# Kernel tuning notes

Measured on AMD Instinct MI355X. Metric: run time of the kernel, lower is better.

## Reference

```python
import jax, jax.numpy as jnp
import numpy as np
import math

B, S, D_IN, D_Q = 4, 2048, 512, 512

def setup_inputs() -> dict:
    key = jax.random.key(0)
    ks = jax.random.split(key, 7)
    s_in = 1.0 / math.sqrt(D_IN)
    x = jax.random.normal(ks[0], (B, S, D_IN), dtype=jnp.float32)
    # nn.Linear-style params: W [out,in], b [out]; uniform(-1/sqrt(in), 1/sqrt(in))
    Wq = jax.random.uniform(ks[1], (D_Q, D_IN), jnp.float32, -s_in, s_in)
    bq = jax.random.uniform(ks[2], (D_Q,), jnp.float32, -s_in, s_in)
    Wk = jax.random.uniform(ks[3], (D_Q, D_IN), jnp.float32, -s_in, s_in)
    bk = jax.random.uniform(ks[4], (D_Q,), jnp.float32, -s_in, s_in)
    Wv = jax.random.uniform(ks[5], (D_Q, D_IN), jnp.float32, -s_in, s_in)
    bv = jax.random.uniform(ks[6], (D_Q,), jnp.float32, -s_in, s_in)
    return {"x": x, "Wq": Wq, "bq": bq, "Wk": Wk, "bk": bk, "Wv": Wv, "bv": bv}

def reference(x, Wq, bq, Wk, bk, Wv, bv):
    # Q/K/V projections: [B,S,D_IN] @ W^T + b -> [B,S,D_Q]
    Q = jnp.einsum('bsi,qi->bsq', x, Wq) + bq
    K = jnp.einsum('bsi,qi->bsq', x, Wk) + bk
    V = jnp.einsum('bsi,qi->bsq', x, Wv) + bv
    scale = 1.0 / math.sqrt(D_Q)
    scores = jnp.einsum('bsq,btq->bst', Q, K) * scale  # [B,S,S]
    attention = jax.nn.softmax(scores, axis=-1)        # 'atten_prob'
    weighted = jnp.einsum('bst,btq->bsq', attention, V)  # 'atten_score'
    return (attention, weighted)
```

## Files before the change

kernel.cpp:

```cpp
#include <hip/hip_runtime.h>
#include <hip/hip_bf16.h>

typedef unsigned short u16;
typedef short bf16x8 __attribute__((ext_vector_type(8)));
typedef float f32x4 __attribute__((ext_vector_type(4)));

#define S_LEN 2048
#define DQ 512
#define NBATCH 4

__device__ __forceinline__ u16 f2bf(float f) {
    __hip_bfloat16 h = __float2bfloat16(f);
    return *reinterpret_cast<u16*>(&h);
}
__device__ __forceinline__ float bf2f(u16 u) {
    unsigned v = ((unsigned)u) << 16;
    union { unsigned u; float f; } c; c.u = v; return c.f;
}

__device__ __forceinline__ void async16(const u16* g, u16* l) {
    __builtin_amdgcn_global_load_lds(
        (__attribute__((address_space(1))) void*)g,
        (__attribute__((address_space(3))) void*)l, 16, 0, 0);
}

__device__ __forceinline__ int xcd_swz(int bid, int chunk) {
    return (bid & 7) * chunk + (bid >> 3);
}

__global__ __launch_bounds__(256) void k_cvt_all(const float* __restrict__ x,
                                                 const float* __restrict__ wq,
                                                 const float* __restrict__ wk,
                                                 const float* __restrict__ wv,
                                                 u16* __restrict__ xb, u16* __restrict__ wb,
                                                 float* __restrict__ sums) {
    int bid = blockIdx.x;
    if (bid >= 4864) {
        int i = (bid - 4864) * 256 + threadIdx.x;
        *(f32x4*)(sums + (size_t)i * 4) = (f32x4)0.0f;
        return;
    }
    const float* src;
    u16* dst;
    int i;
    if (bid < 4096)      { src = x;  dst = xb;          i = bid * 256 + threadIdx.x; }
    else if (bid < 4352) { src = wq; dst = wb;          i = (bid - 4096) * 256 + threadIdx.x; }
    else if (bid < 4608) { src = wk; dst = wb + 262144; i = (bid - 4352) * 256 + threadIdx.x; }
    else                 { src = wv; dst = wb + 524288; i = (bid - 4608) * 256 + threadIdx.x; }
    f32x4 v = *(const f32x4*)(src + (size_t)i * 4);
    ushort4 o;
    o.x = f2bf(v.x); o.y = f2bf(v.y); o.z = f2bf(v.z); o.w = f2bf(v.w);
    *(ushort4*)(dst + (size_t)i * 4) = o;
}

__device__ __forceinline__ void stage_unit(const u16* __restrict__ G, u16* buf,
                                           int kcol, int h, int tid) {
#pragma unroll
    for (int q = 0; q < 2; ++q) {
        int c   = q * 512 + tid;
        int r   = c >> 3;
        int p   = c & 7;
        int lch = p ^ (r & 7);
        async16(G + (size_t)(h * 128 + r) * DQ + kcol + lch * 8,
                buf + h * 8192 + c * 8);
    }
}

__device__ __forceinline__ void gemm256(const u16* __restrict__ A, const u16* __restrict__ B,
                                        u16* ldsA, u16* ldsB, f32x4 acc[8][4], int tid) {
    const int lane = tid & 63;
    const int w    = tid >> 6;
    const int wr   = w >> 2;
    const int wc   = w & 3;
    const int l16  = lane & 15;
    const int quad = lane >> 4;
    const int p0   = quad ^ (l16 & 7);
    const int a0   = (wr * 128 + l16) * 64 + p0 * 8;
    const int a1   = (wr * 128 + l16) * 64 + (p0 ^ 4) * 8;
    const int b0   = (wc * 64 + l16) * 64 + p0 * 8;
    const int b1   = (wc * 64 + l16) * 64 + (p0 ^ 4) * 8;

    stage_unit(A, ldsA, 0, 0, tid);
    stage_unit(A, ldsA, 0, 1, tid);
    stage_unit(B, ldsB, 0, 0, tid);
    stage_unit(B, ldsB, 0, 1, tid);
    __syncthreads();

    for (int kt = 0; kt < 8; ++kt) {
        const u16* rdA = ldsA + (kt & 1) * 16384;
        const u16* rdB = ldsB + (kt & 1) * 16384;
        u16* wrA = ldsA + ((kt + 1) & 1) * 16384;
        u16* wrB = ldsB + ((kt + 1) & 1) * 16384;
        const int  kc = (kt + 1) * 64;
        const bool pf = kt < 7;
        bf16x8 a[4][2], bbf[2][2];

        if (pf) stage_unit(A, wrA, kc, 0, tid);
#pragma unroll
        for (int i = 0; i < 4; ++i) {
            a[i][0] = *(const bf16x8*)(rdA + a0 + i * 1024);
            a[i][1] = *(const bf16x8*)(rdA + a1 + i * 1024);
        }
#pragma unroll
        for (int j = 0; j < 2; ++j) {
            bbf[j][0] = *(const bf16x8*)(rdB + b0 + j * 1024);
            bbf[j][1] = *(const bf16x8*)(rdB + b1 + j * 1024);
        }
        __builtin_amdgcn_s_setprio(1);
#pragma unroll
        for (int i = 0; i < 4; ++i)
#pragma unroll
            for (int j = 0; j < 2; ++j) {
                acc[i][j] = __builtin_amdgcn_mfma_f32_16x16x32_bf16(a[i][0], bbf[j][0], acc[i][j], 0, 0, 0);
                acc[i][j] = __builtin_amdgcn_mfma_f32_16x16x32_bf16(a[i][1], bbf[j][1], acc[i][j], 0, 0, 0);
            }
        __builtin_amdgcn_s_setprio(0);

        if (pf) stage_unit(A, wrA, kc, 1, tid);
#pragma unroll
        for (int j = 0; j < 2; ++j) {
            bbf[j][0] = *(const bf16x8*)(rdB + b0 + (2 + j) * 1024);
            bbf[j][1] = *(const bf16x8*)(rdB + b1 + (2 + j) * 1024);
        }
        __builtin_amdgcn_s_setprio(1);
#pragma unroll
        for (int i = 0; i < 4; ++i)
#pragma unroll
            for (int j = 0; j < 2; ++j) {
                acc[i][2 + j] = __builtin_amdgcn_mfma_f32_16x16x32_bf16(a[i][0], bbf[j][0], acc[i][2 + j], 0, 0, 0);
                acc[i][2 + j] = __builtin_amdgcn_mfma_f32_16x16x32_bf16(a[i][1], bbf[j][1], acc[i][2 + j], 0, 0, 0);
            }
        __builtin_amdgcn_s_setprio(0);

        if (pf) stage_unit(B, wrB, kc, 0, tid);
#pragma unroll
        for (int i = 0; i < 4; ++i) {
            a[i][0] = *(const bf16x8*)(rdA + a0 + (4 + i) * 1024);
            a[i][1] = *(const bf16x8*)(rdA + a1 + (4 + i) * 1024);
        }
        __builtin_amdgcn_s_setprio(1);
#pragma unroll
        for (int i = 0; i < 4; ++i)
#pragma unroll
            for (int j = 0; j < 2; ++j) {
                acc[4 + i][2 + j] = __builtin_amdgcn_mfma_f32_16x16x32_bf16(a[i][0], bbf[j][0], acc[4 + i][2 + j], 0, 0, 0);
                acc[4 + i][2 + j] = __builtin_amdgcn_mfma_f32_16x16x32_bf16(a[i][1], bbf[j][1], acc[4 + i][2 + j], 0, 0, 0);
            }
        __builtin_amdgcn_s_setprio(0);

        if (pf) stage_unit(B, wrB, kc, 1, tid);
#pragma unroll
        for (int j = 0; j < 2; ++j) {
            bbf[j][0] = *(const bf16x8*)(rdB + b0 + j * 1024);
            bbf[j][1] = *(const bf16x8*)(rdB + b1 + j * 1024);
        }
        __builtin_amdgcn_s_setprio(1);
#pragma unroll
        for (int i = 0; i < 4; ++i)
#pragma unroll
            for (int j = 0; j < 2; ++j) {
                acc[4 + i][j] = __builtin_amdgcn_mfma_f32_16x16x32_bf16(a[i][0], bbf[j][0], acc[4 + i][j], 0, 0, 0);
                acc[4 + i][j] = __builtin_amdgcn_mfma_f32_16x16x32_bf16(a[i][1], bbf[j][1], acc[4 + i][j], 0, 0, 0);
            }
        __builtin_amdgcn_s_setprio(0);

        __syncthreads();
    }
}

__global__ __launch_bounds__(512, 2) void k_proj(const u16* __restrict__ xb, const u16* __restrict__ Wb,
                                                 const float* __restrict__ bq, const float* __restrict__ bk,
                                                 const float* __restrict__ bv, u16* __restrict__ out,
                                                 u16* __restrict__ VT) {
    __shared__ __align__(16) u16 lds[65536];
    const int l  = xcd_swz(blockIdx.x, 24);
    const int bx = l & 1;
    const int by = (l >> 1) & 31;
    const int z  = l >> 6;
    const int m0 = by * 256, n0 = bx * 256;
    const u16* A = xb + (size_t)m0 * DQ;
    const u16* B = Wb + (size_t)z * DQ * DQ + (size_t)n0 * DQ;
    const float* bias = (z == 0) ? bq : (z == 1) ? bk : bv;

    f32x4 acc[8][4];
#pragma unroll
    for (int i = 0; i < 8; ++i)
#pragma unroll
        for (int j = 0; j < 4; ++j) acc[i][j] = (f32x4)0.0f;

    const int tid = threadIdx.x;
    gemm256(A, B, lds, lds + 32768, acc, tid);

    const int lane = tid & 63, w = tid >> 6;
    const int wr = w >> 2, wc = w & 3;
    const int l16 = lane & 15, quad = lane >> 4;

    if (z < 2) {
        u16* outz = out + (size_t)z * 8192 * DQ;
#pragma unroll
        for (int j = 0; j < 4; ++j) {
            int gn = n0 + wc * 64 + j * 16 + l16;
            float bv_ = bias[gn];
#pragma unroll
            for (int i = 0; i < 8; ++i)
#pragma unroll
                for (int r = 0; r < 4; ++r) {
                    int gm = m0 + wr * 128 + i * 16 + quad * 4 + r;
                    outz[(size_t)gm * DQ + gn] = f2bf(acc[i][j][r] + bv_);
                }
        }
    } else {
        const int bb_ = m0 >> 11;
        u16* VTb_ = VT + (size_t)bb_ * DQ * S_LEN;
#pragma unroll
        for (int j = 0; j < 4; ++j) {
            int gn = n0 + wc * 64 + j * 16 + l16;
            float bv_ = bias[gn];
#pragma unroll
            for (int i = 0; i < 8; ++i) {
                int t0 = (m0 & 2047) + wr * 128 + i * 16 + quad * 4;
                ushort4 o;
                o.x = f2bf(acc[i][j][0] + bv_);
                o.y = f2bf(acc[i][j][1] + bv_);
                o.z = f2bf(acc[i][j][2] + bv_);
                o.w = f2bf(acc[i][j][3] + bv_);
                *(ushort4*)(VTb_ + (size_t)gn * S_LEN + t0) = o;
            }
        }
    }
}

__global__ __launch_bounds__(512, 2) void k_scores(const u16* __restrict__ Qb, const u16* __restrict__ Kb,
                                                   u16* __restrict__ Pb, float* __restrict__ sums) {
    __shared__ __align__(16) u16 lds[65536];
    const int l  = xcd_swz(blockIdx.x, 32);
    const int bx = l & 7;
    const int by = (l >> 3) & 7;
    const int b  = l >> 6;
    const int m0 = by * 256, n0 = bx * 256;
    const u16* A = Qb + ((size_t)b * S_LEN + m0) * DQ;
    const u16* B = Kb + ((size_t)b * S_LEN + n0) * DQ;

    f32x4 acc[8][4];
#pragma unroll
    for (int i = 0; i < 8; ++i)
#pragma unroll
        for (int j = 0; j < 4; ++j) acc[i][j] = (f32x4)0.0f;

    const int tid = threadIdx.x;
    gemm256(A, B, lds, lds + 32768, acc, tid);

    const float scale = 0.044194173824159216f;
    const int lane = tid & 63, w = tid >> 6;
    const int wr = w >> 2, wc = w & 3;
    const int l16 = lane & 15, quad = lane >> 4;
    u16* prow = Pb + (size_t)(b * S_LEN + m0) * S_LEN;

    float psum[8][4];
#pragma unroll
    for (int i = 0; i < 8; ++i)
#pragma unroll
        for (int r = 0; r < 4; ++r) psum[i][r] = 0.0f;

#pragma unroll
    for (int i = 0; i < 8; ++i)
#pragma unroll
        for (int j = 0; j < 4; ++j)
#pragma unroll
            for (int r = 0; r < 4; ++r) {
                int gm = wr * 128 + i * 16 + quad * 4 + r;
                int gn = n0 + wc * 64 + j * 16 + l16;
                float e = __expf(acc[i][j][r] * scale);
                u16 pbv = f2bf(e);
                prow[(size_t)gm * S_LEN + gn] = pbv;
                psum[i][r] += bf2f(pbv);
            }

    float* sums_row = sums + b * S_LEN + m0 + wr * 128;
#pragma unroll
    for (int i = 0; i < 8; ++i)
#pragma unroll
        for (int r = 0; r < 4; ++r) {
            float v = psum[i][r];
            v += __shfl_xor(v, 1);
            v += __shfl_xor(v, 2);
            v += __shfl_xor(v, 4);
            v += __shfl_xor(v, 8);
            if (l16 == 0) atomicAdd(&sums_row[i * 16 + quad * 4 + r], v);
        }
}

__device__ __forceinline__ void stage_pv(const u16* __restrict__ G, u16* buf,
                                         int kcol, int h, int tid) {
    int c   = tid;
    int r   = c >> 3;
    int p   = c & 7;
    int lch = p ^ (r & 7);
    async16(G + (size_t)(h * 64 + r) * S_LEN + kcol + lch * 8,
            buf + h * 4096 + c * 8);
}

__global__ __launch_bounds__(512, 2) void k_pv(const u16* __restrict__ Pb, const u16* __restrict__ VT,
                                               const float* __restrict__ sums,
                                               float* __restrict__ probs,
                                               float* __restrict__ wout) {
    __shared__ __align__(16) u16 lds[32768];
    u16* ldsA = lds;
    u16* ldsB = lds + 16384;
    const int l  = xcd_swz(blockIdx.x, 32);
    const int bx = l & 3;
    const int by = (l >> 2) & 15;
    const int b  = l >> 6;
    const int m0 = by * 128, n0 = bx * 128;
    const u16* A = Pb + (size_t)(b * S_LEN + m0) * S_LEN;
    const u16* B = VT + (size_t)b * DQ * S_LEN + (size_t)n0 * S_LEN;

    const int tid  = threadIdx.x;
    const int lane = tid & 63;
    const int w    = tid >> 6;
    const int wr   = w >> 2;
    const int wc   = w & 3;
    const int l16  = lane & 15;
    const int quad = lane >> 4;
    const int p0   = quad ^ (l16 & 7);
    const int a0   = (wr * 64 + l16) * 64 + p0 * 8;
    const int a1   = (wr * 64 + l16) * 64 + (p0 ^ 4) * 8;
    const int b0   = (wc * 32 + l16) * 64 + p0 * 8;
    const int b1   = (wc * 32 + l16) * 64 + (p0 ^ 4) * 8;

    f32x4 acc[4][2];
#pragma unroll
    for (int i = 0; i < 4; ++i)
#pragma unroll
        for (int j = 0; j < 2; ++j) acc[i][j] = (f32x4)0.0f;

    stage_pv(A, ldsA, 0, 0, tid);
    stage_pv(A, ldsA, 0, 1, tid);
    stage_pv(B, ldsB, 0, 0, tid);
    stage_pv(B, ldsB, 0, 1, tid);
    __syncthreads();

    for (int kt = 0; kt < 32; ++kt) {
        const u16* rdA = ldsA + (kt & 1) * 8192;
        const u16* rdB = ldsB + (kt & 1) * 8192;
        u16* wrA = ldsA + ((kt + 1) & 1) * 8192;
        u16* wrB = ldsB + ((kt + 1) & 1) * 8192;
        const int  kc = (kt + 1) * 64;
        const bool pf = kt < 31;
        bf16x8 a[4][2], bbf[2];

        if (pf) { stage_pv(A, wrA, kc, 0, tid); stage_pv(A, wrA, kc, 1, tid); }
#pragma unroll
        for (int i = 0; i < 4; ++i) {
            a[i][0] = *(const bf16x8*)(rdA + a0 + i * 1024);
            a[i][1] = *(const bf16x8*)(rdA + a1 + i * 1024);
        }
        bbf[0] = *(const bf16x8*)(rdB + b0);
        bbf[1] = *(const bf16x8*)(rdB + b1);
        __builtin_amdgcn_s_setprio(1);
#pragma unroll
        for (int i = 0; i < 4; ++i) {
            acc[i][0] = __builtin_amdgcn_mfma_f32_16x16x32_bf16(a[i][0], bbf[0], acc[i][0], 0, 0, 0);
            acc[i][0] = __builtin_amdgcn_mfma_f32_16x16x32_bf16(a[i][1], bbf[1], acc[i][0], 0, 0, 0);
        }
        __builtin_amdgcn_s_setprio(0);

        if (pf) { stage_pv(B, wrB, kc, 0, tid); stage_pv(B, wrB, kc, 1, tid); }
        bbf[0] = *(const bf16x8*)(rdB + b0 + 1024);
        bbf[1] = *(const bf16x8*)(rdB + b1 + 1024);
        __builtin_amdgcn_s_setprio(1);
#pragma unroll
        for (int i = 0; i < 4; ++i) {
            acc[i][1] = __builtin_amdgcn_mfma_f32_16x16x32_bf16(a[i][0], bbf[0], acc[i][1], 0, 0, 0);
            acc[i][1] = __builtin_amdgcn_mfma_f32_16x16x32_bf16(a[i][1], bbf[1], acc[i][1], 0, 0, 0);
        }
        __builtin_amdgcn_s_setprio(0);

        __syncthreads();
    }

    float* ldsInv = (float*)lds;
    if (tid < 128) ldsInv[tid] = 1.0f / sums[b * S_LEN + m0 + tid];
    __syncthreads();

    float* outb = wout + (size_t)b * S_LEN * DQ;
#pragma unroll
    for (int i = 0; i < 4; ++i) {
#pragma unroll
        for (int r = 0; r < 4; ++r) {
            int lm = wr * 64 + i * 16 + quad * 4 + r;
            float inv = ldsInv[lm];
#pragma unroll
            for (int j = 0; j < 2; ++j) {
                int gn = n0 + wc * 32 + j * 16 + l16;
                outb[(size_t)(m0 + lm) * DQ + gn] = acc[i][j][r] * inv;
            }
        }
    }

    const u16* Psl = Pb + (size_t)(b * S_LEN + m0) * S_LEN + bx * 512;
    float* Pro = probs + ((size_t)b * S_LEN + m0) * S_LEN + bx * 512;
#pragma unroll
    for (int it = 0; it < 16; ++it) {
        int idx = it * 512 + tid;
        int r  = idx >> 6;
        int cc = (idx & 63) << 3;
        float inv = ldsInv[r];
        bf16x8 vv = *(const bf16x8*)(Psl + (size_t)r * S_LEN + cc);
        f32x4 o0, o1;
        o0.x = bf2f((u16)vv[0]) * inv;
        o0.y = bf2f((u16)vv[1]) * inv;
        o0.z = bf2f((u16)vv[2]) * inv;
        o0.w = bf2f((u16)vv[3]) * inv;
        o1.x = bf2f((u16)vv[4]) * inv;
        o1.y = bf2f((u16)vv[5]) * inv;
        o1.z = bf2f((u16)vv[6]) * inv;
        o1.w = bf2f((u16)vv[7]) * inv;
        float* dst = Pro + (size_t)r * S_LEN + cc;
        *(f32x4*)(dst) = o0;
        *(f32x4*)(dst + 4) = o1;
    }
}

extern "C" void kernel_launch(void* const* d_in, const int* in_sizes, int n_in,
                              void* d_out, int out_size, void* d_ws, size_t ws_size,
                              hipStream_t stream) {
    const float* x  = (const float*)d_in[0];
    const float* Wq = (const float*)d_in[1];
    const float* bq = (const float*)d_in[2];
    const float* Wk = (const float*)d_in[3];
    const float* bk = (const float*)d_in[4];
    const float* Wv = (const float*)d_in[5];
    const float* bv = (const float*)d_in[6];

    char* ws = (char*)d_ws;
    u16* xb  = (u16*)(ws);
    u16* Wb  = (u16*)(ws + 8388608);
    u16* Qb  = (u16*)(ws + 9961472);
    u16* Kb  = (u16*)(ws + 18350080);
    u16* VTb = (u16*)(ws + 35127296);
    u16* Pb  = (u16*)(ws + 43515904);
    float* sums = (float*)(ws + 77070336);
    float* probs = (float*)d_out;
    float* wout  = (float*)d_out + 16777216;

    k_cvt_all<<<4872, 256, 0, stream>>>(x, Wq, Wk, Wv, xb, Wb, sums);
    k_proj<<<192, 512, 0, stream>>>(xb, Wb, bq, bk, bv, Qb, VTb);
    k_scores<<<256, 512, 0, stream>>>(Qb, Kb, Pb, sums);
    k_pv<<<256, 512, 0, stream>>>(Pb, VTb, sums, probs, wout);
}
```

Before: 187.2 us.

## Triple-buffer PV kernel with depth-2 prefetch and move QK stage issues earlier

The P·V kernel moves from double to triple LDS buffering. It prefetches two K-tiles ahead and waits on partial vmcnt counts with raw s_barrier instead of draining all loads at each __syncthreads, to hide global-load latency better. The projection/score GEMM loop now issues all next-tile staging loads in the first two compute phases rather than spreading them over four. The PV kernel's LDS use grows from 64KB to 96KB, which may limit occupancy at 2 blocks per CU, and the hand-counted vmcnt values are fragile.

```diff
diff --git a/kernel.cpp b/kernel.cpp
--- a/kernel.cpp
+++ b/kernel.cpp
@@ -95,7 +95,7 @@
         const bool pf = kt < 7;
         bf16x8 a[4][2], bbf[2][2];
 
-        if (pf) stage_unit(A, wrA, kc, 0, tid);
+        if (pf) { stage_unit(A, wrA, kc, 0, tid); stage_unit(A, wrA, kc, 1, tid); }
 #pragma unroll
         for (int i = 0; i < 4; ++i) {
             a[i][0] = *(const bf16x8*)(rdA + a0 + i * 1024);
@@ -116,7 +116,7 @@
             }
         __builtin_amdgcn_s_setprio(0);
 
-        if (pf) stage_unit(A, wrA, kc, 1, tid);
+        if (pf) { stage_unit(B, wrB, kc, 0, tid); stage_unit(B, wrB, kc, 1, tid); }
 #pragma unroll
         for (int j = 0; j < 2; ++j) {
             bbf[j][0] = *(const bf16x8*)(rdB + b0 + (2 + j) * 1024);
@@ -132,7 +132,6 @@
             }
         __builtin_amdgcn_s_setprio(0);
 
-        if (pf) stage_unit(B, wrB, kc, 0, tid);
 #pragma unroll
         for (int i = 0; i < 4; ++i) {
             a[i][0] = *(const bf16x8*)(rdA + a0 + (4 + i) * 1024);
@@ -148,7 +147,6 @@
             }
         __builtin_amdgcn_s_setprio(0);
 
-        if (pf) stage_unit(B, wrB, kc, 1, tid);
 #pragma unroll
         for (int j = 0; j < 2; ++j) {
             bbf[j][0] = *(const bf16x8*)(rdB + b0 + j * 1024);
@@ -304,9 +302,9 @@
                                                const float* __restrict__ sums,
                                                float* __restrict__ probs,
                                                float* __restrict__ wout) {
-    __shared__ __align__(16) u16 lds[32768];
+    __shared__ __align__(16) u16 lds[49152];
     u16* ldsA = lds;
-    u16* ldsB = lds + 16384;
+    u16* ldsB = lds + 24576;
     const int l  = xcd_swz(blockIdx.x, 32);
     const int bx = l & 3;
     const int by = (l >> 2) & 15;
@@ -334,22 +332,30 @@
 #pragma unroll
         for (int j = 0; j < 2; ++j) acc[i][j] = (f32x4)0.0f;
 
-    stage_pv(A, ldsA, 0, 0, tid);
-    stage_pv(A, ldsA, 0, 1, tid);
-    stage_pv(B, ldsB, 0, 0, tid);
-    stage_pv(B, ldsB, 0, 1, tid);
-    __syncthreads();
-
+    stage_pv(A, ldsA, 0, 0, tid);          stage_pv(A, ldsA, 0, 1, tid);
+    stage_pv(B, ldsB, 0, 0, tid);          stage_pv(B, ldsB, 0, 1, tid);
+    stage_pv(A, ldsA + 8192, 64, 0, tid);  stage_pv(A, ldsA + 8192, 64, 1, tid);
+    stage_pv(B, ldsB + 8192, 64, 0, tid);  stage_pv(B, ldsB + 8192, 64, 1, tid);
+    asm volatile("s_waitcnt vmcnt(4)" ::: "memory");
+    __builtin_amdgcn_s_barrier();
+    __builtin_amdgcn_sched_barrier(0);
+
+    int rb = 0;
     for (int kt = 0; kt < 32; ++kt) {
-        const u16* rdA = ldsA + (kt & 1) * 8192;
-        const u16* rdB = ldsB + (kt & 1) * 8192;
-        u16* wrA = ldsA + ((kt + 1) & 1) * 8192;
-        u16* wrB = ldsB + ((kt + 1) & 1) * 8192;
-        const int  kc = (kt + 1) * 64;
-        const bool pf = kt < 31;
+        const u16* rdA = ldsA + rb * 8192;
+        const u16* rdB = ldsB + rb * 8192;
+        if (kt < 30) {
+            int wbi = rb >= 1 ? rb - 1 : 2;
+            u16* wA = ldsA + wbi * 8192;
+            u16* wB = ldsB + wbi * 8192;
+            const int kc = (kt + 2) * 64;
+            stage_pv(A, wA, kc, 0, tid);
+            stage_pv(A, wA, kc, 1, tid);
+            stage_pv(B, wB, kc, 0, tid);
+            stage_pv(B, wB, kc, 1, tid);
+        }
+
         bf16x8 a[4][2], bbf[2];
-
-        if (pf) { stage_pv(A, wrA, kc, 0, tid); stage_pv(A, wrA, kc, 1, tid); }
 #pragma unroll
         for (int i = 0; i < 4; ++i) {
             a[i][0] = *(const bf16x8*)(rdA + a0 + i * 1024);
@@ -365,7 +371,6 @@
         }
         __builtin_amdgcn_s_setprio(0);
 
-        if (pf) { stage_pv(B, wrB, kc, 0, tid); stage_pv(B, wrB, kc, 1, tid); }
         bbf[0] = *(const bf16x8*)(rdB + b0 + 1024);
         bbf[1] = *(const bf16x8*)(rdB + b1 + 1024);
         __builtin_amdgcn_s_setprio(1);
@@ -376,7 +381,13 @@
         }
         __builtin_amdgcn_s_setprio(0);
 
-        __syncthreads();
+        if (kt < 31) {
+            if (kt < 30) asm volatile("s_waitcnt vmcnt(4)" ::: "memory");
+            else         asm volatile("s_waitcnt vmcnt(0)" ::: "memory");
+            __builtin_amdgcn_s_barrier();
+            __builtin_amdgcn_sched_barrier(0);
+        }
+        rb = (rb == 2) ? 0 : rb + 1;
     }
 
     float* ldsInv = (float*)lds;
```

New measurement: 182.2 us. 1.03x faster.
